# Kernel tuning notes

Measured on AMD Instinct MI355X. Metric: run time of the kernel, lower is better.

## Reference

```python
import jax, jax.numpy as jnp
import numpy as np

B, S, D = 4, 4096, 1024
H, HEAD_DIM = 16, 192  # head_dim split into q/k/v of 64 each


def setup_inputs() -> dict:
    key = jax.random.key(0)
    k1, k2 = jax.random.split(key)
    x = jax.random.normal(k1, (B, S, D), dtype=jnp.float32)
    qkv_kernel = jax.random.normal(k2, (D, H, HEAD_DIM), dtype=jnp.float32) * (1.0 / np.sqrt(D))
    qkv_bias = jnp.zeros((H, HEAD_DIM), dtype=jnp.float32)
    return {"x": x, "qkv_kernel": qkv_kernel, "qkv_bias": qkv_bias}


def reference(x, qkv_kernel, qkv_bias):
    # DenseGeneral: [B,S,D] x [D,H,HEAD_DIM] -> [B,S,H,HEAD_DIM]
    qkv = jnp.einsum('bsd,dhf->bshf', x, qkv_kernel) + qkv_bias
    q, k, v = jnp.split(qkv, 3, axis=-1)  # each [B,S,H,64]
    # Faithful to source layout: einsum '...hqd,...hkd' batches over (B,S) and
    # attends across the HEAD axis. With H <= block_size the blockwise loop in
    # the source collapses to this single full softmax over heads.
    scale = 1.0 / jnp.sqrt(jnp.asarray(HEAD_DIM, dtype=q.dtype))  # sqrt(self.head_dim)
    scores = jnp.einsum('bshd,bsgd->bshg', q, k) * scale  # [B,S,H,H]
    weights = jax.nn.softmax(scores, axis=-1)
    out = jnp.einsum('bshg,bsgd->bshd', weights, v)  # [B,S,H,64]
    return out
```

## Files before the change

kernel.cpp:

```cpp
#include <hip/hip_runtime.h>
#include <cstdint>
#include <cstddef>

typedef unsigned short u16;
typedef __attribute__((ext_vector_type(8))) short bf16x8;
typedef __attribute__((ext_vector_type(4))) float f32x4;

__device__ inline float bl(uint32_t u){ union{float f;uint32_t i;}c; c.i = u<<16; return c.f; }
__device__ inline float bh(uint32_t u){ union{float f;uint32_t i;}c; c.i = u & 0xFFFF0000u; return c.f; }
__device__ inline u16 f2bu(float f){
  union{float f;uint32_t u;} c; c.f=f;
  uint32_t u=c.u;
  return (u16)((u + 0x7FFFu + ((u>>16)&1u))>>16);
}

#define GLOAD_LDS16(g, l) __builtin_amdgcn_global_load_lds( \
    (__attribute__((address_space(1))) void*)(g), \
    (__attribute__((address_space(3))) void*)(l), 16, 0, 0)
#define BAR() do{ asm volatile("" ::: "memory"); __builtin_amdgcn_s_barrier(); asm volatile("" ::: "memory"); }while(0)

__global__ __launch_bounds__(256) void k_conv(const float* __restrict__ X,
                                              u16* __restrict__ Xb,
                                              const float* __restrict__ W,
                                              u16* __restrict__ Wt){
  __shared__ float t[32][33];
  int b = blockIdx.x;
  if (b < 2048){
    int i = b*256 + threadIdx.x;
    for (; i < 4194304; i += 2048*256){
      float4 v = ((const float4*)X)[i];
      ushort4 o;
      o.x=f2bu(v.x); o.y=f2bu(v.y); o.z=f2bu(v.z); o.w=f2bu(v.w);
      ((ushort4*)Xb)[i] = o;
    }
  } else {
    int bb = b - 2048;
    int n0 = (bb % 96)*32, k0 = (bb / 96)*32;
    int tx = threadIdx.x & 31, ty = threadIdx.x >> 5;
    #pragma unroll
    for (int i=0;i<32;i+=8)
      t[ty+i][tx] = W[(size_t)(k0+ty+i)*3072 + n0+tx];
    __syncthreads();
    #pragma unroll
    for (int i=0;i<32;i+=8)
      Wt[(size_t)(n0+ty+i)*1024 + k0+tx] = f2bu(t[tx][ty+i]);
  }
}

__global__ __launch_bounds__(512, 1) void k_gemm2(const u16* __restrict__ Xb,
                                                  const u16* __restrict__ Wt,
                                                  const float* __restrict__ bias,
                                                  u16* __restrict__ Q){
  __shared__ __align__(16) u16 L[81920];
  const int K = 1024, N = 3072, NT = 32;
  int b = blockIdx.x;
  int swz = (b & 7)*96 + (b >> 3);
  int bm = swz / 12, bn = swz % 12;
  int m0 = bm*256, n0 = bn*256;
  int tid = threadIdx.x, w = tid>>6, lane = tid&63, lr = lane&15, lk = lane>>4;
  int wm = w>>2, wn = w&3;

  f32x4 acc[8][4];
  #pragma unroll
  for (int i=0;i<8;i++)
    #pragma unroll
    for (int j=0;j<4;j++)
      acc[i][j] = (f32x4){0.f,0.f,0.f,0.f};

  int grow = tid>>2;
  int gcol = ((((tid&3)*16) ^ (((tid>>3)&1)<<4) ^ (((tid>>4)&1)<<5)) >> 1);
  const u16* gA0 = Xb + (size_t)(m0 + grow)*K + gcol;
  const u16* gA1 = Xb + (size_t)(m0 + 128 + grow)*K + gcol;
  const u16* gB0 = Wt + (size_t)(n0 + grow)*K + gcol;
  const u16* gB1 = Wt + (size_t)(n0 + 128 + grow)*K + gcol;

#define STG(j) do{ int bf=(j)%5, kof=(j)*32; \
    GLOAD_LDS16(gA0+kof, &L[((bf*4+0)<<12) + tid*8]); \
    GLOAD_LDS16(gA1+kof, &L[((bf*4+1)<<12) + tid*8]); \
    GLOAD_LDS16(gB0+kof, &L[((bf*4+2)<<12) + tid*8]); \
    GLOAD_LDS16(gB1+kof, &L[((bf*4+3)<<12) + tid*8]); }while(0)

  const char* Lb = (const char*)L;
  int colx = (lk*16) ^ (((lr>>1)&3)*16);
  int arow = lr*64 + colx;
  int brow = ((wn&1)*64 + lr)*64 + colx;

#define TILE_BODY(bufidx) do{ \
    int Abase = ((bufidx)*4 + wm) << 13; \
    int Bbase = ((bufidx)*4 + 2 + (wn>>1)) << 13; \
    bf16x8 a0,a1,a2,a3,a4,a5,a6,a7, b0,b1,b2,b3; \
    a0 = *(const bf16x8*)(Lb + Abase + 0*1024 + arow); \
    a1 = *(const bf16x8*)(Lb + Abase + 1*1024 + arow); \
    a2 = *(const bf16x8*)(Lb + Abase + 2*1024 + arow); \
    a3 = *(const bf16x8*)(Lb + Abase + 3*1024 + arow); \
    a4 = *(const bf16x8*)(Lb + Abase + 4*1024 + arow); \
    a5 = *(const bf16x8*)(Lb + Abase + 5*1024 + arow); \
    a6 = *(const bf16x8*)(Lb + Abase + 6*1024 + arow); \
    a7 = *(const bf16x8*)(Lb + Abase + 7*1024 + arow); \
    b0 = *(const bf16x8*)(Lb + Bbase + 0*1024 + brow); \
    b1 = *(const bf16x8*)(Lb + Bbase + 1*1024 + brow); \
    b2 = *(const bf16x8*)(Lb + Bbase + 2*1024 + brow); \
    b3 = *(const bf16x8*)(Lb + Bbase + 3*1024 + brow); \
    __builtin_amdgcn_s_setprio(1); \
    acc[0][0] = __builtin_amdgcn_mfma_f32_16x16x32_bf16(a0, b0, acc[0][0], 0,0,0); \
    acc[0][1] = __builtin_amdgcn_mfma_f32_16x16x32_bf16(a0, b1, acc[0][1], 0,0,0); \
    acc[0][2] = __builtin_amdgcn_mfma_f32_16x16x32_bf16(a0, b2, acc[0][2], 0,0,0); \
    acc[0][3] = __builtin_amdgcn_mfma_f32_16x16x32_bf16(a0, b3, acc[0][3], 0,0,0); \
    acc[1][0] = __builtin_amdgcn_mfma_f32_16x16x32_bf16(a1, b0, acc[1][0], 0,0,0); \
    acc[1][1] = __builtin_amdgcn_mfma_f32_16x16x32_bf16(a1, b1, acc[1][1], 0,0,0); \
    acc[1][2] = __builtin_amdgcn_mfma_f32_16x16x32_bf16(a1, b2, acc[1][2], 0,0,0); \
    acc[1][3] = __builtin_amdgcn_mfma_f32_16x16x32_bf16(a1, b3, acc[1][3], 0,0,0); \
    acc[2][0] = __builtin_amdgcn_mfma_f32_16x16x32_bf16(a2, b0, acc[2][0], 0,0,0); \
    acc[2][1] = __builtin_amdgcn_mfma_f32_16x16x32_bf16(a2, b1, acc[2][1], 0,0,0); \
    acc[2][2] = __builtin_amdgcn_mfma_f32_16x16x32_bf16(a2, b2, acc[2][2], 0,0,0); \
    acc[2][3] = __builtin_amdgcn_mfma_f32_16x16x32_bf16(a2, b3, acc[2][3], 0,0,0); \
    acc[3][0] = __builtin_amdgcn_mfma_f32_16x16x32_bf16(a3, b0, acc[3][0], 0,0,0); \
    acc[3][1] = __builtin_amdgcn_mfma_f32_16x16x32_bf16(a3, b1, acc[3][1], 0,0,0); \
    acc[3][2] = __builtin_amdgcn_mfma_f32_16x16x32_bf16(a3, b2, acc[3][2], 0,0,0); \
    acc[3][3] = __builtin_amdgcn_mfma_f32_16x16x32_bf16(a3, b3, acc[3][3], 0,0,0); \
    acc[4][0] = __builtin_amdgcn_mfma_f32_16x16x32_bf16(a4, b0, acc[4][0], 0,0,0); \
    acc[4][1] = __builtin_amdgcn_mfma_f32_16x16x32_bf16(a4, b1, acc[4][1], 0,0,0); \
    acc[4][2] = __builtin_amdgcn_mfma_f32_16x16x32_bf16(a4, b2, acc[4][2], 0,0,0); \
    acc[4][3] = __builtin_amdgcn_mfma_f32_16x16x32_bf16(a4, b3, acc[4][3], 0,0,0); \
    acc[5][0] = __builtin_amdgcn_mfma_f32_16x16x32_bf16(a5, b0, acc[5][0], 0,0,0); \
    acc[5][1] = __builtin_amdgcn_mfma_f32_16x16x32_bf16(a5, b1, acc[5][1], 0,0,0); \
    acc[5][2] = __builtin_amdgcn_mfma_f32_16x16x32_bf16(a5, b2, acc[5][2], 0,0,0); \
    acc[5][3] = __builtin_amdgcn_mfma_f32_16x16x32_bf16(a5, b3, acc[5][3], 0,0,0); \
    acc[6][0] = __builtin_amdgcn_mfma_f32_16x16x32_bf16(a6, b0, acc[6][0], 0,0,0); \
    acc[6][1] = __builtin_amdgcn_mfma_f32_16x16x32_bf16(a6, b1, acc[6][1], 0,0,0); \
    acc[6][2] = __builtin_amdgcn_mfma_f32_16x16x32_bf16(a6, b2, acc[6][2], 0,0,0); \
    acc[6][3] = __builtin_amdgcn_mfma_f32_16x16x32_bf16(a6, b3, acc[6][3], 0,0,0); \
    acc[7][0] = __builtin_amdgcn_mfma_f32_16x16x32_bf16(a7, b0, acc[7][0], 0,0,0); \
    acc[7][1] = __builtin_amdgcn_mfma_f32_16x16x32_bf16(a7, b1, acc[7][1], 0,0,0); \
    acc[7][2] = __builtin_amdgcn_mfma_f32_16x16x32_bf16(a7, b2, acc[7][2], 0,0,0); \
    acc[7][3] = __builtin_amdgcn_mfma_f32_16x16x32_bf16(a7, b3, acc[7][3], 0,0,0); \
    __builtin_amdgcn_s_setprio(0); }while(0)

  STG(0); STG(1); STG(2);
  asm volatile("s_waitcnt vmcnt(4)" ::: "memory");
  __builtin_amdgcn_sched_barrier(0);
  BAR();

  for (int t = 0; t < NT; t += 2){
    if (t+3 < NT) STG(t+3);
    TILE_BODY(t%5);
    if (t+4 < NT) STG(t+4);
    TILE_BODY((t+1)%5);
    asm volatile("s_waitcnt lgkmcnt(0)" ::: "memory");
    if      (t+4 < NT) { asm volatile("s_waitcnt vmcnt(4)" ::: "memory"); }
    else if (t+2 < NT) { asm volatile("s_waitcnt vmcnt(0)" ::: "memory"); }
    __builtin_amdgcn_sched_barrier(0);
    BAR();
  }
#undef STG
#undef TILE_BODY

  {
    u16* reg = &L[w*8192];
    #pragma unroll
    for (int nf=0; nf<4; ++nf){
      int col = nf*16 + lr;
      float bv = bias[n0 + wn*64 + col];
      #pragma unroll
      for (int mi=0; mi<8; ++mi){
        #pragma unroll
        for (int r=0;r<4;r++){
          int rr = mi*16 + lk*4 + r;
          reg[rr*64 + (col ^ ((rr&7)<<3))] = f2bu(acc[mi][nf][r] + bv);
        }
      }
    }
    asm volatile("s_waitcnt lgkmcnt(0)" ::: "memory");
    BAR();
    int co = (tid&31)*8;
    int rgn_c = co>>6;
    int c6 = co&63;
    #pragma unroll
    for (int p=0; p<16; ++p){
      int rI = p*16 + (tid>>5);
      int wreg = ((rI>>7)<<2) + rgn_c;
      int rr = rI & 127;
      const u16* src = &L[wreg*8192 + rr*64 + (c6 ^ ((rr&7)<<3))];
      uint4 v = *(const uint4*)src;
      *(uint4*)&Q[(size_t)(m0+rI)*N + n0 + co] = v;
    }
  }
}

__device__ inline void load16fb(const u16* p, float* f){
  uint4 a = ((const uint4*)p)[0], b4 = ((const uint4*)p)[1];
  f[0]=bl(a.x);  f[1]=bh(a.x);  f[2]=bl(a.y);  f[3]=bh(a.y);
  f[4]=bl(a.z);  f[5]=bh(a.z);  f[6]=bl(a.w);  f[7]=bh(a.w);
  f[8]=bl(b4.x); f[9]=bh(b4.x); f[10]=bl(b4.y);f[11]=bh(b4.y);
  f[12]=bl(b4.z);f[13]=bh(b4.z);f[14]=bl(b4.w);f[15]=bh(b4.w);
}

__global__ __launch_bounds__(256) void k_attn(const u16* __restrict__ Qkv,
                                              float* __restrict__ out){
  __shared__ __align__(16) u16 sm[4][3072];
  int w = threadIdx.x>>6, lane = threadIdx.x&63;
  int token = blockIdx.x*4 + w;
  const uint4* src = (const uint4*)(Qkv + (size_t)token*3072);
  uint4* dst = (uint4*)&sm[w][0];
  for (int i = lane; i < 384; i += 64) dst[i] = src[i];
  __syncthreads();

  int h = lane>>2, dq = lane&3;
  const u16* base = &sm[w][0];
  float qf[16];
  load16fb(base + h*192 + dq*16, qf);

  const float scale = 0.07216878364870323f;
  float s[16];
  #pragma unroll
  for (int g=0; g<16; ++g){
    float kf[16];
    load16fb(base + g*192 + 64 + dq*16, kf);
    float a = 0.f;
    #pragma unroll
    for (int j=0;j<16;j++) a += qf[j]*kf[j];
    a += __shfl_xor(a, 1);
    a += __shfl_xor(a, 2);
    s[g] = a * scale;
  }
  float mx = s[0];
  #pragma unroll
  for (int g=1; g<16; ++g) mx = fmaxf(mx, s[g]);
  float sum = 0.f;
  #pragma unroll
  for (int g=0; g<16; ++g){ s[g] = __expf(s[g]-mx); sum += s[g]; }
  float inv = 1.f/sum;

  float o[16];
  #pragma unroll
  for (int j=0;j<16;j++) o[j] = 0.f;
  #pragma unroll
  for (int g=0; g<16; ++g){
    float wg = s[g]*inv;
    float vf[16];
    load16fb(base + g*192 + 128 + dq*16, vf);
    #pragma unroll
    for (int j=0;j<16;j++) o[j] += wg*vf[j];
  }
  float* op = out + (size_t)token*1024 + h*64 + dq*16;
  #pragma unroll
  for (int i=0;i<4;i++)
    ((float4*)op)[i] = make_float4(o[i*4], o[i*4+1], o[i*4+2], o[i*4+3]);
}

__global__ __launch_bounds__(256) void k_fallback(const float* __restrict__ X,
                                                  const float* __restrict__ W,
                                                  const float* __restrict__ bias,
                                                  float* __restrict__ out){
  int token = blockIdx.x;
  __shared__ float xs[1024];
  __shared__ float qkvs[3072];
  __shared__ float ss[16][16];
  __shared__ float ww[16][16];
  for (int i=threadIdx.x; i<1024; i+=256) xs[i] = X[(size_t)token*1024 + i];
  __syncthreads();
  for (int n=threadIdx.x; n<3072; n+=256){
    float acc = bias[n];
    for (int k=0;k<1024;k++) acc += xs[k]*W[(size_t)k*3072 + n];
    qkvs[n] = acc;
  }
  __syncthreads();
  {
    int t = threadIdx.x, h = t>>4, g = t&15;
    float a = 0.f;
    for (int d=0; d<64; d++) a += qkvs[h*192 + d]*qkvs[g*192 + 64 + d];
    ss[h][g] = a * 0.07216878364870323f;
  }
  __syncthreads();
  if (threadIdx.x < 16){
    int hh = threadIdx.x;
    float m = -1e30f;
    for (int g=0;g<16;g++) m = fmaxf(m, ss[hh][g]);
    float sum = 0.f;
    for (int g=0;g<16;g++){ float e = __expf(ss[hh][g]-m); ww[hh][g]=e; sum+=e; }
    float inv = 1.f/sum;
    for (int g=0;g<16;g++) ww[hh][g] *= inv;
  }
  __syncthreads();
  for (int i=threadIdx.x; i<1024; i+=256){
    int h = i>>6, d = i&63;
    float a = 0.f;
    for (int g=0;g<16;g++) a += ww[h][g]*qkvs[g*192 + 128 + d];
    out[(size_t)token*1024 + i] = a;
  }
}

extern "C" void kernel_launch(void* const* d_in, const int* in_sizes, int n_in,
                              void* d_out, int out_size, void* d_ws, size_t ws_size,
                              hipStream_t stream){
  const float* x    = (const float*)d_in[0];
  const float* wk   = (const float*)d_in[1];
  const float* bias = (const float*)d_in[2];
  float* out = (float*)d_out;

  const size_t offW = 33554432;
  const size_t offQ = offW + 6291456;
  const size_t need = offQ + (size_t)16384*3072*2;

  if (ws_size >= need){
    u16* Xb = (u16*)d_ws;
    u16* Wt = (u16*)((char*)d_ws + offW);
    u16* Q  = (u16*)((char*)d_ws + offQ);
    k_conv  <<<5120, 256, 0, stream>>>(x, Xb, wk, Wt);
    k_gemm2 <<<768, 512, 0, stream>>>(Xb, Wt, bias, Q);
    k_attn  <<<4096, 256, 0, stream>>>(Q, out);
  } else {
    k_fallback<<<16384, 256, 0, stream>>>(x, wk, bias, out);
  }
}
```

Measured before the change: 190.9 us.

## Use 4 waves per GEMM block with 128x128 per-wave tiles

Result: slower. 315.8 us (+65.4%).

```diff
diff --git a/kernel.cpp b/kernel.cpp
--- a/kernel.cpp
+++ b/kernel.cpp
@@ -47,7 +47,7 @@
   }
 }
 
-__global__ __launch_bounds__(512, 1) void k_gemm2(const u16* __restrict__ Xb,
+__global__ __launch_bounds__(256, 1) void k_gemm2(const u16* __restrict__ Xb,
                                                   const u16* __restrict__ Wt,
                                                   const float* __restrict__ bias,
                                                   u16* __restrict__ Q){
@@ -58,86 +58,53 @@
   int bm = swz / 12, bn = swz % 12;
   int m0 = bm*256, n0 = bn*256;
   int tid = threadIdx.x, w = tid>>6, lane = tid&63, lr = lane&15, lk = lane>>4;
-  int wm = w>>2, wn = w&3;
-
-  f32x4 acc[8][4];
+  int wm = w>>1, wn = w&1;
+
+  f32x4 acc[8][8];
   #pragma unroll
   for (int i=0;i<8;i++)
     #pragma unroll
-    for (int j=0;j<4;j++)
+    for (int j=0;j<8;j++)
       acc[i][j] = (f32x4){0.f,0.f,0.f,0.f};
 
   int grow = tid>>2;
   int gcol = ((((tid&3)*16) ^ (((tid>>3)&1)<<4) ^ (((tid>>4)&1)<<5)) >> 1);
-  const u16* gA0 = Xb + (size_t)(m0 + grow)*K + gcol;
-  const u16* gA1 = Xb + (size_t)(m0 + 128 + grow)*K + gcol;
-  const u16* gB0 = Wt + (size_t)(n0 + grow)*K + gcol;
-  const u16* gB1 = Wt + (size_t)(n0 + 128 + grow)*K + gcol;
+  const u16* gA = Xb + (size_t)(m0 + grow)*K + gcol;
+  const u16* gB = Wt + (size_t)(n0 + grow)*K + gcol;
+  const size_t r64 = (size_t)64*K;
 
 #define STG(j) do{ int bf=(j)%5, kof=(j)*32; \
-    GLOAD_LDS16(gA0+kof, &L[((bf*4+0)<<12) + tid*8]); \
-    GLOAD_LDS16(gA1+kof, &L[((bf*4+1)<<12) + tid*8]); \
-    GLOAD_LDS16(gB0+kof, &L[((bf*4+2)<<12) + tid*8]); \
-    GLOAD_LDS16(gB1+kof, &L[((bf*4+3)<<12) + tid*8]); }while(0)
+    GLOAD_LDS16(gA + kof,          &L[((bf*4+0)<<12) + tid*8]); \
+    GLOAD_LDS16(gA + r64 + kof,    &L[((bf*4+0)<<12) + 2048 + tid*8]); \
+    GLOAD_LDS16(gA + 2*r64 + kof,  &L[((bf*4+1)<<12) + tid*8]); \
+    GLOAD_LDS16(gA + 3*r64 + kof,  &L[((bf*4+1)<<12) + 2048 + tid*8]); \
+    GLOAD_LDS16(gB + kof,          &L[((bf*4+2)<<12) + tid*8]); \
+    GLOAD_LDS16(gB + r64 + kof,    &L[((bf*4+2)<<12) + 2048 + tid*8]); \
+    GLOAD_LDS16(gB + 2*r64 + kof,  &L[((bf*4+3)<<12) + tid*8]); \
+    GLOAD_LDS16(gB + 3*r64 + kof,  &L[((bf*4+3)<<12) + 2048 + tid*8]); }while(0)
 
   const char* Lb = (const char*)L;
   int colx = (lk*16) ^ (((lr>>1)&3)*16);
-  int arow = lr*64 + colx;
-  int brow = ((wn&1)*64 + lr)*64 + colx;
+  int frow = lr*64 + colx;
 
 #define TILE_BODY(bufidx) do{ \
     int Abase = ((bufidx)*4 + wm) << 13; \
-    int Bbase = ((bufidx)*4 + 2 + (wn>>1)) << 13; \
-    bf16x8 a0,a1,a2,a3,a4,a5,a6,a7, b0,b1,b2,b3; \
-    a0 = *(const bf16x8*)(Lb + Abase + 0*1024 + arow); \
-    a1 = *(const bf16x8*)(Lb + Abase + 1*1024 + arow); \
-    a2 = *(const bf16x8*)(Lb + Abase + 2*1024 + arow); \
-    a3 = *(const bf16x8*)(Lb + Abase + 3*1024 + arow); \
-    a4 = *(const bf16x8*)(Lb + Abase + 4*1024 + arow); \
-    a5 = *(const bf16x8*)(Lb + Abase + 5*1024 + arow); \
-    a6 = *(const bf16x8*)(Lb + Abase + 6*1024 + arow); \
-    a7 = *(const bf16x8*)(Lb + Abase + 7*1024 + arow); \
-    b0 = *(const bf16x8*)(Lb + Bbase + 0*1024 + brow); \
-    b1 = *(const bf16x8*)(Lb + Bbase + 1*1024 + brow); \
-    b2 = *(const bf16x8*)(Lb + Bbase + 2*1024 + brow); \
-    b3 = *(const bf16x8*)(Lb + Bbase + 3*1024 + brow); \
+    int Bbase = ((bufidx)*4 + 2 + wn) << 13; \
+    bf16x8 af[8], bfr[8]; \
+    _Pragma("unroll") \
+    for (int i=0;i<8;i++) af[i]  = *(const bf16x8*)(Lb + Abase + i*1024 + frow); \
+    _Pragma("unroll") \
+    for (int i=0;i<8;i++) bfr[i] = *(const bf16x8*)(Lb + Bbase + i*1024 + frow); \
     __builtin_amdgcn_s_setprio(1); \
-    acc[0][0] = __builtin_amdgcn_mfma_f32_16x16x32_bf16(a0, b0, acc[0][0], 0,0,0); \
-    acc[0][1] = __builtin_amdgcn_mfma_f32_16x16x32_bf16(a0, b1, acc[0][1], 0,0,0); \
-    acc[0][2] = __builtin_amdgcn_mfma_f32_16x16x32_bf16(a0, b2, acc[0][2], 0,0,0); \
-    acc[0][3] = __builtin_amdgcn_mfma_f32_16x16x32_bf16(a0, b3, acc[0][3], 0,0,0); \
-    acc[1][0] = __builtin_amdgcn_mfma_f32_16x16x32_bf16(a1, b0, acc[1][0], 0,0,0); \
-    acc[1][1] = __builtin_amdgcn_mfma_f32_16x16x32_bf16(a1, b1, acc[1][1], 0,0,0); \
-    acc[1][2] = __builtin_amdgcn_mfma_f32_16x16x32_bf16(a1, b2, acc[1][2], 0,0,0); \
-    acc[1][3] = __builtin_amdgcn_mfma_f32_16x16x32_bf16(a1, b3, acc[1][3], 0,0,0); \
-    acc[2][0] = __builtin_amdgcn_mfma_f32_16x16x32_bf16(a2, b0, acc[2][0], 0,0,0); \
-    acc[2][1] = __builtin_amdgcn_mfma_f32_16x16x32_bf16(a2, b1, acc[2][1], 0,0,0); \
-    acc[2][2] = __builtin_amdgcn_mfma_f32_16x16x32_bf16(a2, b2, acc[2][2], 0,0,0); \
-    acc[2][3] = __builtin_amdgcn_mfma_f32_16x16x32_bf16(a2, b3, acc[2][3], 0,0,0); \
-    acc[3][0] = __builtin_amdgcn_mfma_f32_16x16x32_bf16(a3, b0, acc[3][0], 0,0,0); \
-    acc[3][1] = __builtin_amdgcn_mfma_f32_16x16x32_bf16(a3, b1, acc[3][1], 0,0,0); \
-    acc[3][2] = __builtin_amdgcn_mfma_f32_16x16x32_bf16(a3, b2, acc[3][2], 0,0,0); \
-    acc[3][3] = __builtin_amdgcn_mfma_f32_16x16x32_bf16(a3, b3, acc[3][3], 0,0,0); \
-    acc[4][0] = __builtin_amdgcn_mfma_f32_16x16x32_bf16(a4, b0, acc[4][0], 0,0,0); \
-    acc[4][1] = __builtin_amdgcn_mfma_f32_16x16x32_bf16(a4, b1, acc[4][1], 0,0,0); \
-    acc[4][2] = __builtin_amdgcn_mfma_f32_16x16x32_bf16(a4, b2, acc[4][2], 0,0,0); \
-    acc[4][3] = __builtin_amdgcn_mfma_f32_16x16x32_bf16(a4, b3, acc[4][3], 0,0,0); \
-    acc[5][0] = __builtin_amdgcn_mfma_f32_16x16x32_bf16(a5, b0, acc[5][0], 0,0,0); \
-    acc[5][1] = __builtin_amdgcn_mfma_f32_16x16x32_bf16(a5, b1, acc[5][1], 0,0,0); \
-    acc[5][2] = __builtin_amdgcn_mfma_f32_16x16x32_bf16(a5, b2, acc[5][2], 0,0,0); \
-    acc[5][3] = __builtin_amdgcn_mfma_f32_16x16x32_bf16(a5, b3, acc[5][3], 0,0,0); \
-    acc[6][0] = __builtin_amdgcn_mfma_f32_16x16x32_bf16(a6, b0, acc[6][0], 0,0,0); \
-    acc[6][1] = __builtin_amdgcn_mfma_f32_16x16x32_bf16(a6, b1, acc[6][1], 0,0,0); \
-    acc[6][2] = __builtin_amdgcn_mfma_f32_16x16x32_bf16(a6, b2, acc[6][2], 0,0,0); \
-    acc[6][3] = __builtin_amdgcn_mfma_f32_16x16x32_bf16(a6, b3, acc[6][3], 0,0,0); \
-    acc[7][0] = __builtin_amdgcn_mfma_f32_16x16x32_bf16(a7, b0, acc[7][0], 0,0,0); \
-    acc[7][1] = __builtin_amdgcn_mfma_f32_16x16x32_bf16(a7, b1, acc[7][1], 0,0,0); \
-    acc[7][2] = __builtin_amdgcn_mfma_f32_16x16x32_bf16(a7, b2, acc[7][2], 0,0,0); \
-    acc[7][3] = __builtin_amdgcn_mfma_f32_16x16x32_bf16(a7, b3, acc[7][3], 0,0,0); \
+    _Pragma("unroll") \
+    for (int mi=0;mi<8;mi++) \
+      _Pragma("unroll") \
+      for (int ni=0;ni<8;ni++) \
+        acc[mi][ni] = __builtin_amdgcn_mfma_f32_16x16x32_bf16(af[mi], bfr[ni], acc[mi][ni], 0,0,0); \
     __builtin_amdgcn_s_setprio(0); }while(0)
 
   STG(0); STG(1); STG(2);
-  asm volatile("s_waitcnt vmcnt(4)" ::: "memory");
+  asm volatile("s_waitcnt vmcnt(8)" ::: "memory");
   __builtin_amdgcn_sched_barrier(0);
   BAR();
 
@@ -147,7 +114,7 @@
     if (t+4 < NT) STG(t+4);
     TILE_BODY((t+1)%5);
     asm volatile("s_waitcnt lgkmcnt(0)" ::: "memory");
-    if      (t+4 < NT) { asm volatile("s_waitcnt vmcnt(4)" ::: "memory"); }
+    if      (t+4 < NT) { asm volatile("s_waitcnt vmcnt(8)" ::: "memory"); }
     else if (t+2 < NT) { asm volatile("s_waitcnt vmcnt(0)" ::: "memory"); }
     __builtin_amdgcn_sched_barrier(0);
     BAR();
@@ -156,31 +123,30 @@
 #undef TILE_BODY
 
   {
-    u16* reg = &L[w*8192];
-    #pragma unroll
-    for (int nf=0; nf<4; ++nf){
-      int col = nf*16 + lr;
-      float bv = bias[n0 + wn*64 + col];
+    u16* reg = &L[w*16384];
+    #pragma unroll
+    for (int ni=0; ni<8; ++ni){
+      int col = ni*16 + lr;
+      float bv = bias[n0 + wn*128 + col];
       #pragma unroll
       for (int mi=0; mi<8; ++mi){
         #pragma unroll
         for (int r=0;r<4;r++){
           int rr = mi*16 + lk*4 + r;
-          reg[rr*64 + (col ^ ((rr&7)<<3))] = f2bu(acc[mi][nf][r] + bv);
+          reg[rr*128 + (col ^ ((rr&15)<<3))] = f2bu(acc[mi][ni][r] + bv);
         }
       }
     }
     asm volatile("s_waitcnt lgkmcnt(0)" ::: "memory");
     BAR();
     int co = (tid&31)*8;
-    int rgn_c = co>>6;
-    int c6 = co&63;
-    #pragma unroll
-    for (int p=0; p<16; ++p){
-      int rI = p*16 + (tid>>5);
-      int wreg = ((rI>>7)<<2) + rgn_c;
+    #pragma unroll
+    for (int p=0; p<32; ++p){
+      int rI = p*8 + (tid>>5);
+      int wreg = ((rI>>7)<<1) + (co>>7);
       int rr = rI & 127;
-      const u16* src = &L[wreg*8192 + rr*64 + (c6 ^ ((rr&7)<<3))];
+      int cc = co & 127;
+      const u16* src = &L[wreg*16384 + rr*128 + (cc ^ ((rr&15)<<3))];
       uint4 v = *(const uint4*)src;
       *(uint4*)&Q[(size_t)(m0+rI)*N + n0 + co] = v;
     }
@@ -307,7 +273,7 @@
     u16* Wt = (u16*)((char*)d_ws + offW);
     u16* Q  = (u16*)((char*)d_ws + offQ);
     k_conv  <<<5120, 256, 0, stream>>>(x, Xb, wk, Wt);
-    k_gemm2 <<<768, 512, 0, stream>>>(Xb, Wt, bias, Q);
+    k_gemm2 <<<768, 256, 0, stream>>>(Xb, Wt, bias, Q);
     k_attn  <<<4096, 256, 0, stream>>>(Q, out);
   } else {
     k_fallback<<<16384, 256, 0, stream>>>(x, wk, bias, out);
```
